# Kernel tuning notes

Hardware: AMD Instinct MI355X
Metric: run time of the kernel (lower is better)

Reference implementation:

```python
import jax, jax.numpy as jnp
import numpy as np

H, HD, CHUNK = 16, 64, 128


def _rotary(x):
    # x: (B,H,N,d); rotary_embedding_torch default: interleaved pairs, theta=10000
    N, d = x.shape[-2], x.shape[-1]
    inv_freq = 1.0 / (10000.0 ** (jnp.arange(0, d, 2, dtype=jnp.float32) / d))
    ang = jnp.arange(N, dtype=jnp.float32)[:, None] * inv_freq[None, :]  # (N, d/2)
    ang = jnp.repeat(ang, 2, axis=-1)  # (N, d), each freq repeated twice
    cos, sin = jnp.cos(ang), jnp.sin(ang)
    x1, x2 = x[..., 0::2], x[..., 1::2]
    xr = jnp.stack([-x2, x1], axis=-1).reshape(x.shape)  # rotate_half (interleaved)
    return x * cos + xr * sin


def _split_heads(t, B, N):
    return t.reshape(B, N, H, HD).transpose(0, 2, 1, 3)  # (B,H,N,Hd)


def _chunked(Q, KK, VK):
    # chunk-parallel linear-attention recurrence: per-token outer products,
    # intra-chunk cumsum, carried state across chunks, Frobenius normalization.
    B, h, N, d = Q.shape
    nc = N // CHUNK

    def to_chunks(t):
        return t.reshape(B, h, nc, CHUNK, d).transpose(2, 0, 1, 3, 4)  # (nc,B,h,c,d)

    S0 = jnp.eye(d, dtype=Q.dtype) * jnp.sqrt(jnp.float32(d))
    S0 = jnp.broadcast_to(S0, (B, h, d, d))

    def step(SK_state, inp):
        q, kk, vk = inp  # (B,h,c,d)
        ok = jnp.einsum('bhni,bhnj->bhnij', kk, vk)            # outer products
        SK = jnp.cumsum(ok, axis=2) + SK_state[:, :, None]      # prefix-sum + carry
        norm = jnp.sqrt(jnp.sum(SK * SK, axis=(-2, -1), keepdims=True)) + 1e-8
        SKn = SK / norm                                         # Frobenius-normalized
        y = jnp.einsum('bhni,bhnji->bhnj', q, SKn)              # q @ SK^T per token
        return SK[:, :, -1], y

    _, ys = jax.lax.scan(step, S0, (to_chunks(Q), to_chunks(KK), to_chunks(VK)))
    return ys.transpose(1, 2, 0, 3, 4).reshape(B, h, N, d)


def setup_inputs():
    key = jax.random.key(0)
    ks = jax.random.split(key, 5)
    B, N, D = 2, 2048, 1024
    X = jax.random.normal(ks[0], (B, N, D), jnp.float32)
    w_qkv = jax.random.normal(ks[1], (D, 3 * H * HD), jnp.float32) * 0.02
    w_kvkv = jax.random.normal(ks[2], (D, 4 * H * HD), jnp.float32) * 0.02
    w_out = jax.random.normal(ks[3], (H * HD, D), jnp.float32) * 0.02
    b_out = jnp.zeros((D,), jnp.float32)
    return {"X": X, "w_qkv": w_qkv, "w_kvkv": w_kvkv, "w_out": w_out, "b_out": b_out}


def reference(X, w_qkv, w_kvkv, w_out, b_out):
    B, N, D = X.shape
    q, k, v = jnp.split(X @ w_qkv, 3, axis=-1)
    Q = _split_heads(q, B, N)
    K = _split_heads(k, B, N)
    V = _split_heads(v, B, N)
    kk, vk, _kv, _vv = jnp.split(X @ w_kvkv, 4, axis=-1)
    KK = _split_heads(kk, B, N)
    VK = _split_heads(vk, B, N)
    # NOTE: the SV branch (KV, VV) in the original is returned by the chunked fn
    # but never used by forward's output, so it is dead code for the fwd result.
    Qn = _chunked(Q, KK, VK)
    Qr = _rotary(Qn)
    Kr = _rotary(K)
    scale = 1.0 / jnp.sqrt(jnp.float32(HD))
    scores = jnp.einsum('bhqd,bhkd->bhqk', Qr, Kr) * scale
    mask = jnp.tril(jnp.ones((N, N), dtype=bool))
    scores = jnp.where(mask, scores, -jnp.inf)
    attn = jax.nn.softmax(scores, axis=-1)
    out = jnp.einsum('bhqk,bhkd->bhqd', attn, V)
    out = out.transpose(0, 2, 1, 3).reshape(B, N, H * HD)
    return out @ w_out + b_out
```

## Files before the change

kernel.cpp:

```cpp
#include <hip/hip_runtime.h>

typedef unsigned int u32;
typedef unsigned short u16;
typedef __attribute__((ext_vector_type(8))) __bf16 bf16x8;
typedef __attribute__((ext_vector_type(4))) float f32x4;

constexpr int NH = 16;
constexpr int HDM = 64;
constexpr int NSQ = 2048;
constexpr int KD = 1024;
constexpr int BHT = 32;

__device__ __forceinline__ u16 f2bf(float f) {
  u32 u = __float_as_uint(f);
  u += 0x7fffu + ((u >> 16) & 1u);
  return (u16)(u >> 16);
}
__device__ __forceinline__ float bf2f(u16 h) {
  return __uint_as_float(((u32)h) << 16);
}

__device__ __forceinline__ void gl_lds16(const u16* g, u16* l) {
  __builtin_amdgcn_global_load_lds(
      (const __attribute__((address_space(1))) u32*)g,
      (__attribute__((address_space(3))) u32*)l, 16, 0, 0);
}

__device__ __forceinline__ bf16x8 ldf(const u16* b, int row, int cb, int rs) {
  return *(const bf16x8*)((const char*)b + row * rs + ((cb * 16) ^ ((row & 7) << 4)));
}

__global__ void k_f32_to_bf16(const float* __restrict__ src, u16* __restrict__ dst, int n4) {
  int i = blockIdx.x * 256 + threadIdx.x;
  if (i < n4) {
    float4 v = ((const float4*)src)[i];
    ushort4 o;
    o.x = f2bf(v.x); o.y = f2bf(v.y); o.z = f2bf(v.z); o.w = f2bf(v.w);
    ((ushort4*)dst)[i] = o;
  }
}

__global__ void k_transpose_bf16(const float* __restrict__ src, int srcld,
                                 u16* __restrict__ dst, int dstld) {
  __shared__ float tile[64][65];
  int ct = blockIdx.x * 64, kt = blockIdx.y * 64;
  int lc = threadIdx.x & 63, rg = threadIdx.x >> 6;
#pragma unroll
  for (int i = 0; i < 16; ++i) {
    int kl = rg * 16 + i;
    tile[kl][lc] = src[(size_t)(kt + kl) * srcld + ct + lc];
  }
  __syncthreads();
#pragma unroll
  for (int i = 0; i < 16; ++i) {
    int cl = rg * 16 + i;
    dst[(size_t)(ct + cl) * dstld + kt + lc] = f2bf(tile[lc][cl]);
  }
}

template <int MODE>
__device__ __forceinline__ void gemm_stage(const u16* __restrict__ A, const u16* __restrict__ Bt,
                                           u16* Albuf, u16* Blbuf, int mt, int nt, int kt,
                                           int w, int lane) {
#pragma unroll
  for (int i = 0; i < 2; ++i) {
    int ob = (w * 2 + i) * 1024 + lane * 16;
    int row = ob >> 6;
    int ke = (ob & 63) >> 1;
    const u16* ga;
    if (MODE == 0) {
      ga = A + (size_t)(mt * 128 + row) * KD + kt * 32 + ke;
    } else {
      int grow = mt * 128 + row;
      int k = kt * 32 + ke;
      ga = A + ((size_t)((grow >> 11) * NH + (k >> 6)) * NSQ + (grow & 2047)) * HDM + (k & 63);
    }
    gl_lds16(ga, Albuf + (w * 2 + i) * 512);
    const u16* gb = Bt + (size_t)(nt * 128 + row) * KD + kt * 32 + ke;
    gl_lds16(gb, Blbuf + (w * 2 + i) * 512);
  }
}

__device__ __forceinline__ void gemm_compute(const u16* Albuf, const u16* Blbuf,
                                             f32x4 acc[4][4], int wr, int wc, int g, int q) {
  bf16x8 af[4], bfr[4];
#pragma unroll
  for (int m = 0; m < 4; ++m)
    af[m] = *(const bf16x8*)(Albuf + (wr * 64 + m * 16 + q) * 32 + g * 8);
#pragma unroll
  for (int n = 0; n < 4; ++n)
    bfr[n] = *(const bf16x8*)(Blbuf + (wc * 64 + n * 16 + q) * 32 + g * 8);
#pragma unroll
  for (int m = 0; m < 4; ++m)
#pragma unroll
    for (int n = 0; n < 4; ++n)
      acc[m][n] = __builtin_amdgcn_mfma_f32_16x16x32_bf16(af[m], bfr[n], acc[m][n], 0, 0, 0);
}

template <int MODE>
__global__ __launch_bounds__(256) void k_gemm(const u16* __restrict__ A, const u16* __restrict__ Bt,
                                              u16* __restrict__ o0, u16* __restrict__ o1,
                                              u16* __restrict__ o2, u16* __restrict__ o3,
                                              u16* __restrict__ o4,
                                              const float* __restrict__ bias,
                                              float* __restrict__ Cout) {
  __shared__ __align__(16) u16 Al[2][4096];
  __shared__ __align__(16) u16 Bl[2][4096];
  int nt = blockIdx.x, mt = blockIdx.y;
  int tid = threadIdx.x, w = tid >> 6, lane = tid & 63;
  int g = lane >> 4, q = lane & 15, wr = w >> 1, wc = w & 1;
  f32x4 acc[4][4];
#pragma unroll
  for (int m = 0; m < 4; ++m)
#pragma unroll
    for (int n = 0; n < 4; ++n) acc[m][n] = (f32x4){0.f, 0.f, 0.f, 0.f};

  gemm_stage<MODE>(A, Bt, Al[0], Bl[0], mt, nt, 0, w, lane);
  __syncthreads();
  int cur = 0;
  for (int kt = 1; kt < 32; ++kt) {
    gemm_stage<MODE>(A, Bt, Al[cur ^ 1], Bl[cur ^ 1], mt, nt, kt, w, lane);
    gemm_compute(Al[cur], Bl[cur], acc, wr, wc, g, q);
    __syncthreads();
    cur ^= 1;
  }
  gemm_compute(Al[cur], Bl[cur], acc, wr, wc, g, q);

  if (MODE == 0) {
#pragma unroll
    for (int nf = 0; nf < 4; ++nf) {
      int c = nt * 128 + wc * 64 + nf * 16 + q;
      if (c >= 2048 && c < 3072) {
        int rem = c - 2048;
        int hh = rem >> 6, dd = rem & 63;
#pragma unroll
        for (int mf = 0; mf < 4; ++mf)
#pragma unroll
          for (int r = 0; r < 4; ++r) {
            int row = mt * 128 + wr * 64 + mf * 16 + g * 4 + r;
            int b = row >> 11, nn = row & 2047;
            o2[((size_t)(b * NH + hh) * HDM + dd) * NSQ + nn] = f2bf(acc[mf][nf][r]);
          }
      } else {
        u16* dst; int rem;
        if (c < 1024)      { dst = o0; rem = c; }
        else if (c < 2048) { dst = o1; rem = c - 1024; }
        else if (c < 4096) { dst = o3; rem = c - 3072; }
        else               { dst = o4; rem = c - 4096; }
        size_t hoff = (size_t)(rem >> 6) * NSQ * HDM + (rem & 63);
#pragma unroll
        for (int mf = 0; mf < 4; ++mf)
#pragma unroll
          for (int r = 0; r < 4; ++r) {
            int row = mt * 128 + wr * 64 + mf * 16 + g * 4 + r;
            int b = row >> 11, nn = row & 2047;
            dst[(size_t)b * NH * NSQ * HDM + hoff + (size_t)nn * HDM] = f2bf(acc[mf][nf][r]);
          }
      }
    }
  } else {
#pragma unroll
    for (int nf = 0; nf < 4; ++nf) {
      int c = nt * 128 + wc * 64 + nf * 16 + q;
      float bv = bias[c];
#pragma unroll
      for (int mf = 0; mf < 4; ++mf)
#pragma unroll
        for (int r = 0; r < 4; ++r) {
          int row = mt * 128 + wr * 64 + mf * 16 + g * 4 + r;
          Cout[(size_t)row * 1024 + c] = acc[mf][nf][r] + bv;
        }
    }
  }
}

__global__ void k_rotary(const u16* __restrict__ src, u16* __restrict__ dst, float scale) {
  int idx = blockIdx.x * 256 + threadIdx.x;
  if (idx >= BHT * NSQ * 32) return;
  int i = idx & 31;
  int n = (idx >> 5) & 2047;
  int bh = idx >> 16;
  float th = (float)n * exp2f(-(float)i * (13.287712379549449f / 32.0f));
  float s, c;
  sincosf(th, &s, &c);
  size_t base = ((size_t)bh * NSQ + n) * HDM + 2 * i;
  float x1 = bf2f(src[base]), x2 = bf2f(src[base + 1]);
  dst[base]     = f2bf((x1 * c - x2 * s) * scale);
  dst[base + 1] = f2bf((x2 * c + x1 * s) * scale);
}

__global__ __launch_bounds__(256) void k_chunk_outer(const u16* __restrict__ Kk,
                                                     const u16* __restrict__ Vk,
                                                     float* __restrict__ Mc) {
  int bhc = blockIdx.x;
  __shared__ float kk[128][64];
  __shared__ float vv[128][64];
  int tid = threadIdx.x;
  size_t base = ((size_t)(bhc >> 4) * NSQ + (size_t)(bhc & 15) * 128) * HDM;
  for (int i = tid; i < 2048; i += 256) {
    int r = i >> 4, c4 = (i & 15) * 4;
    ushort4 a = ((const ushort4*)(Kk + base))[i];
    kk[r][c4] = bf2f(a.x); kk[r][c4 + 1] = bf2f(a.y); kk[r][c4 + 2] = bf2f(a.z); kk[r][c4 + 3] = bf2f(a.w);
    ushort4 b = ((const ushort4*)(Vk + base))[i];
    vv[r][c4] = bf2f(b.x); vv[r][c4 + 1] = bf2f(b.y); vv[r][c4 + 2] = bf2f(b.z); vv[r][c4 + 3] = bf2f(b.w);
  }
  __syncthreads();
  int i0 = (tid >> 4) * 4, j0 = (tid & 15) * 4;
  float a2[4][4];
#pragma unroll
  for (int di = 0; di < 4; ++di)
#pragma unroll
    for (int dj = 0; dj < 4; ++dj) a2[di][dj] = 0.f;
  for (int m = 0; m < 128; ++m) {
    float ka[4], vb[4];
#pragma unroll
    for (int d = 0; d < 4; ++d) { ka[d] = kk[m][i0 + d]; vb[d] = vv[m][j0 + d]; }
#pragma unroll
    for (int di = 0; di < 4; ++di)
#pragma unroll
      for (int dj = 0; dj < 4; ++dj) a2[di][dj] += ka[di] * vb[dj];
  }
  float* out = Mc + (size_t)bhc * 4096;
#pragma unroll
  for (int di = 0; di < 4; ++di) {
    float4 v = make_float4(a2[di][0], a2[di][1], a2[di][2], a2[di][3]);
    *(float4*)(out + (i0 + di) * 64 + j0) = v;
  }
}

__global__ void k_chunk_prefix(const float* __restrict__ Mc, float* __restrict__ Sst) {
  int bh = blockIdx.x;
  int tid = threadIdx.x;
  int i0 = (tid >> 4) * 4, j0 = (tid & 15) * 4;
  float S[4][4];
#pragma unroll
  for (int di = 0; di < 4; ++di)
#pragma unroll
    for (int dj = 0; dj < 4; ++dj) S[di][dj] = ((i0 + di) == (j0 + dj)) ? 8.0f : 0.0f;
  for (int c = 0; c < 16; ++c) {
    size_t o = ((size_t)bh * 16 + c) * 4096;
#pragma unroll
    for (int di = 0; di < 4; ++di) {
      float4 v = make_float4(S[di][0], S[di][1], S[di][2], S[di][3]);
      *(float4*)(Sst + o + (i0 + di) * 64 + j0) = v;
      float4 mv = *(const float4*)(Mc + o + (i0 + di) * 64 + j0);
      S[di][0] += mv.x; S[di][1] += mv.y; S[di][2] += mv.z; S[di][3] += mv.w;
    }
  }
}

__global__ __launch_bounds__(256) void k_chunk_norm(const u16* __restrict__ Kk,
                                                    const u16* __restrict__ Vk,
                                                    const float* __restrict__ Sst,
                                                    float* __restrict__ Invn) {
  __shared__ __align__(16) u16 KkL[128 * 64];
  __shared__ __align__(16) u16 VkL[128 * 64];
  __shared__ __align__(16) u16 SL[64 * 64];
  __shared__ float prebuf[128][2];
  __shared__ float bilbuf[128][2];
  __shared__ float sc[128];
  __shared__ float red[4];
  int bhc = blockIdx.x;
  int tid = threadIdx.x, w = tid >> 6, lane = tid & 63;
  int g = lane >> 4, q = lane & 15;
  size_t base = (size_t)bhc * 8192;

  for (int ic = tid; ic < 1024; ic += 256) {
    int row = ic >> 3, cb = ic & 7;
    int off = row * 128 + ((cb * 16) ^ ((row & 7) << 4));
    *(uint4*)((char*)KkL + off) = ((const uint4*)(Kk + base))[ic];
    *(uint4*)((char*)VkL + off) = ((const uint4*)(Vk + base))[ic];
  }
  float ss = 0.f;
  const float4* Sg = (const float4*)(Sst + (size_t)bhc * 4096);
  for (int i = tid; i < 1024; i += 256) {
    float4 v = Sg[i];
    ss += v.x * v.x + v.y * v.y + v.z * v.z + v.w * v.w;
    int row = i >> 4, c8 = (i & 15) * 8;
    u32 lo = (u32)f2bf(v.x) | ((u32)f2bf(v.y) << 16);
    u32 hi = (u32)f2bf(v.z) | ((u32)f2bf(v.w) << 16);
    *(uint2*)((char*)SL + row * 128 + (c8 ^ ((row & 7) << 4))) = make_uint2(lo, hi);
  }
#pragma unroll
  for (int d = 1; d < 64; d <<= 1) ss += __shfl_xor(ss, d);
  if (lane == 0) red[w] = ss;
  __syncthreads();

  int wr = w >> 1, wc = w & 1;
  bf16x8 ka[4][2], va[4][2];
#pragma unroll
  for (int mf = 0; mf < 4; ++mf)
#pragma unroll
    for (int ks = 0; ks < 2; ++ks) {
      ka[mf][ks] = ldf(KkL, wr * 64 + mf * 16 + q, ks * 4 + g, 128);
      va[mf][ks] = ldf(VkL, wr * 64 + mf * 16 + q, ks * 4 + g, 128);
    }

  float pracc[4][4];
#pragma unroll
  for (int mf = 0; mf < 4; ++mf)
#pragma unroll
    for (int r = 0; r < 4; ++r) pracc[mf][r] = 0.f;
  for (int pf = 0; pf < 4; ++pf) {
    bf16x8 kb0 = ldf(KkL, wc * 64 + pf * 16 + q, g, 128);
    bf16x8 kb1 = ldf(KkL, wc * 64 + pf * 16 + q, 4 + g, 128);
    bf16x8 vb0 = ldf(VkL, wc * 64 + pf * 16 + q, g, 128);
    bf16x8 vb1 = ldf(VkL, wc * 64 + pf * 16 + q, 4 + g, 128);
#pragma unroll
    for (int mf = 0; mf < 4; ++mf) {
      f32x4 a1 = (f32x4){0.f, 0.f, 0.f, 0.f}, b1 = (f32x4){0.f, 0.f, 0.f, 0.f};
      a1 = __builtin_amdgcn_mfma_f32_16x16x32_bf16(ka[mf][0], kb0, a1, 0, 0, 0);
      a1 = __builtin_amdgcn_mfma_f32_16x16x32_bf16(ka[mf][1], kb1, a1, 0, 0, 0);
      b1 = __builtin_amdgcn_mfma_f32_16x16x32_bf16(va[mf][0], vb0, b1, 0, 0, 0);
      b1 = __builtin_amdgcn_mfma_f32_16x16x32_bf16(va[mf][1], vb1, b1, 0, 0, 0);
#pragma unroll
      for (int r = 0; r < 4; ++r) {
        int m = wr * 64 + mf * 16 + g * 4 + r;
        int p = wc * 64 + pf * 16 + q;
        float gv = a1[r] * b1[r];
        float coef = (p < m) ? 1.f : ((p == m) ? 0.5f : 0.f);
        pracc[mf][r] += coef * gv;
      }
    }
  }
#pragma unroll
  for (int mf = 0; mf < 4; ++mf)
#pragma unroll
    for (int r = 0; r < 4; ++r) {
      float v = pracc[mf][r];
      v += __shfl_xor(v, 1); v += __shfl_xor(v, 2); v += __shfl_xor(v, 4); v += __shfl_xor(v, 8);
      pracc[mf][r] = v;
    }
  if (q == 0) {
#pragma unroll
    for (int mf = 0; mf < 4; ++mf)
#pragma unroll
      for (int r = 0; r < 4; ++r) prebuf[wr * 64 + mf * 16 + g * 4 + r][wc] = pracc[mf][r];
  }

  float bacc[4][4];
#pragma unroll
  for (int mf = 0; mf < 4; ++mf)
#pragma unroll
    for (int r = 0; r < 4; ++r) bacc[mf][r] = 0.f;
  for (int jf = 0; jf < 2; ++jf) {
    bf16x8 sb0 = ldf(SL, wc * 32 + jf * 16 + q, g, 128);
    bf16x8 sb1 = ldf(SL, wc * 32 + jf * 16 + q, 4 + g, 128);
#pragma unroll
    for (int mf = 0; mf < 4; ++mf) {
      f32x4 u = (f32x4){0.f, 0.f, 0.f, 0.f};
      u = __builtin_amdgcn_mfma_f32_16x16x32_bf16(va[mf][0], sb0, u, 0, 0, 0);
      u = __builtin_amdgcn_mfma_f32_16x16x32_bf16(va[mf][1], sb1, u, 0, 0, 0);
#pragma unroll
      for (int r = 0; r < 4; ++r) {
        int m = wr * 64 + mf * 16 + g * 4 + r;
        int j = wc * 32 + jf * 16 + q;
        float kkv = bf2f(*(const u16*)((const char*)KkL + m * 128 + ((j * 2) ^ ((m & 7) << 4))));
        bacc[mf][r] += u[r] * kkv;
      }
    }
  }
#pragma unroll
  for (int mf = 0; mf < 4; ++mf)
#pragma unroll
    for (int r = 0; r < 4; ++r) {
      float v = bacc[mf][r];
      v += __shfl_xor(v, 1); v += __shfl_xor(v, 2); v += __shfl_xor(v, 4); v += __shfl_xor(v, 8);
      bacc[mf][r] = v;
    }
  if (q == 0) {
#pragma unroll
    for (int mf = 0; mf < 4; ++mf)
#pragma unroll
      for (int r = 0; r < 4; ++r) bilbuf[wr * 64 + mf * 16 + g * 4 + r][wc] = bacc[mf][r];
  }
  __syncthreads();

  if (tid < 128)
    sc[tid] = 2.f * (prebuf[tid][0] + prebuf[tid][1] + bilbuf[tid][0] + bilbuf[tid][1]);
  __syncthreads();
  for (int off = 1; off < 128; off <<= 1) {
    float add = 0.f;
    if (tid < 128 && tid >= off) add = sc[tid - off];
    __syncthreads();
    if (tid < 128) sc[tid] += add;
    __syncthreads();
  }
  if (tid < 128) {
    float n0 = red[0] + red[1] + red[2] + red[3];
    float cum = n0 + sc[tid];
    Invn[(size_t)bhc * 128 + tid] = 1.f / (sqrtf(cum) + 1e-8f);
  }
}

__global__ __launch_bounds__(256) void k_chunk_yv2(const u16* __restrict__ Qb,
                                                   const u16* __restrict__ Kk,
                                                   const u16* __restrict__ Vk,
                                                   const float* __restrict__ Sst,
                                                   const float* __restrict__ Invn,
                                                   u16* __restrict__ Qn) {
  __shared__ __align__(16) u16 QL[128 * 64];
  __shared__ __align__(16) u16 WL[128 * 64];
  __shared__ __align__(16) u16 SL[64 * 64];
  __shared__ __align__(16) u16 PL[128 * 128];
  __shared__ float inv[128];
  int bhc = blockIdx.x;
  int tid = threadIdx.x, w = tid >> 6, lane = tid & 63;
  int g = lane >> 4, q = lane & 15;
  size_t base = (size_t)bhc * 8192;

  for (int ic = tid; ic < 1024; ic += 256) {
    int row = ic >> 3, cb = ic & 7;
    int off = row * 128 + ((cb * 16) ^ ((row & 7) << 4));
    *(uint4*)((char*)QL + off) = ((const uint4*)(Qb + base))[ic];
    *(uint4*)((char*)WL + off) = ((const uint4*)(Vk + base))[ic];
  }
  const float4* Sg = (const float4*)(Sst + (size_t)bhc * 4096);
  for (int i = tid; i < 1024; i += 256) {
    float4 v = Sg[i];
    int row = i >> 4, c8 = (i & 15) * 8;
    u32 lo = (u32)f2bf(v.x) | ((u32)f2bf(v.y) << 16);
    u32 hi = (u32)f2bf(v.z) | ((u32)f2bf(v.w) << 16);
    *(uint2*)((char*)SL + row * 128 + (c8 ^ ((row & 7) << 4))) = make_uint2(lo, hi);
  }
  if (tid < 128) inv[tid] = Invn[(size_t)bhc * 128 + tid];
  __syncthreads();

  int wr = w >> 1, wc = w & 1;
  f32x4 pacc[4][4];
#pragma unroll
  for (int mf = 0; mf < 4; ++mf)
#pragma unroll
    for (int nf = 0; nf < 4; ++nf) pacc[mf][nf] = (f32x4){0.f, 0.f, 0.f, 0.f};
#pragma unroll
  for (int ks = 0; ks < 2; ++ks) {
    bf16x8 av[4], bq[4];
#pragma unroll
    for (int mf = 0; mf < 4; ++mf) av[mf] = ldf(WL, wr * 64 + mf * 16 + q, ks * 4 + g, 128);
#pragma unroll
    for (int nf = 0; nf < 4; ++nf) bq[nf] = ldf(QL, wc * 64 + nf * 16 + q, ks * 4 + g, 128);
#pragma unroll
    for (int mf = 0; mf < 4; ++mf)
#pragma unroll
      for (int nf = 0; nf < 4; ++nf)
        pacc[mf][nf] = __builtin_amdgcn_mfma_f32_16x16x32_bf16(av[mf], bq[nf], pacc[mf][nf], 0, 0, 0);
  }
#pragma unroll
  for (int mf = 0; mf < 4; ++mf)
#pragma unroll
    for (int nf = 0; nf < 4; ++nf) {
      int m0 = wr * 64 + mf * 16 + g * 4;
      int n = wc * 64 + nf * 16 + q;
      float v0 = (m0 + 0 <= n) ? pacc[mf][nf][0] : 0.f;
      float v1 = (m0 + 1 <= n) ? pacc[mf][nf][1] : 0.f;
      float v2 = (m0 + 2 <= n) ? pacc[mf][nf][2] : 0.f;
      float v3 = (m0 + 3 <= n) ? pacc[mf][nf][3] : 0.f;
      u32 lo = (u32)f2bf(v0) | ((u32)f2bf(v1) << 16);
      u32 hi = (u32)f2bf(v2) | ((u32)f2bf(v3) << 16);
      *(uint2*)((char*)PL + n * 256 + ((m0 * 2) ^ ((n & 7) << 4))) = make_uint2(lo, hi);
    }
  __syncthreads();
  for (int i = tid; i < 2048; i += 256) {
    int r = i >> 4, c4 = (i & 15) * 4;
    ushort4 kv = ((const ushort4*)(Kk + base))[i];
    *(u16*)((char*)WL + (c4 + 0) * 256 + ((r * 2) ^ (((c4 + 0) & 7) << 4))) = kv.x;
    *(u16*)((char*)WL + (c4 + 1) * 256 + ((r * 2) ^ (((c4 + 1) & 7) << 4))) = kv.y;
    *(u16*)((char*)WL + (c4 + 2) * 256 + ((r * 2) ^ (((c4 + 2) & 7) << 4))) = kv.z;
    *(u16*)((char*)WL + (c4 + 3) * 256 + ((r * 2) ^ (((c4 + 3) & 7) << 4))) = kv.w;
  }
  __syncthreads();

  f32x4 yacc[4][2];
#pragma unroll
  for (int nf = 0; nf < 4; ++nf)
#pragma unroll
    for (int jf = 0; jf < 2; ++jf) yacc[nf][jf] = (f32x4){0.f, 0.f, 0.f, 0.f};
#pragma unroll
  for (int ks = 0; ks < 2; ++ks) {
    bf16x8 aq[4], bs[2];
#pragma unroll
    for (int nf = 0; nf < 4; ++nf) aq[nf] = ldf(QL, wr * 64 + nf * 16 + q, ks * 4 + g, 128);
#pragma unroll
    for (int jf = 0; jf < 2; ++jf) bs[jf] = ldf(SL, wc * 32 + jf * 16 + q, ks * 4 + g, 128);
#pragma unroll
    for (int nf = 0; nf < 4; ++nf)
#pragma unroll
      for (int jf = 0; jf < 2; ++jf)
        yacc[nf][jf] = __builtin_amdgcn_mfma_f32_16x16x32_bf16(aq[nf], bs[jf], yacc[nf][jf], 0, 0, 0);
  }
#pragma unroll
  for (int ks = 0; ks < 4; ++ks) {
    bf16x8 ap[4], bk[2];
#pragma unroll
    for (int nf = 0; nf < 4; ++nf) ap[nf] = ldf(PL, wr * 64 + nf * 16 + q, ks * 4 + g, 256);
#pragma unroll
    for (int jf = 0; jf < 2; ++jf) bk[jf] = ldf(WL, wc * 32 + jf * 16 + q, ks * 4 + g, 256);
#pragma unroll
    for (int nf = 0; nf < 4; ++nf)
#pragma unroll
      for (int jf = 0; jf < 2; ++jf)
        yacc[nf][jf] = __builtin_amdgcn_mfma_f32_16x16x32_bf16(ap[nf], bk[jf], yacc[nf][jf], 0, 0, 0);
  }
#pragma unroll
  for (int nf = 0; nf < 4; ++nf)
#pragma unroll
    for (int jf = 0; jf < 2; ++jf)
#pragma unroll
      for (int r = 0; r < 4; ++r) {
        int n = wr * 64 + nf * 16 + g * 4 + r;
        int j = wc * 32 + jf * 16 + q;
        Qn[base + (size_t)n * 64 + j] = f2bf(yacc[nf][jf][r] * inv[n]);
      }
}

__global__ __launch_bounds__(512) void k_attn2(const u16* __restrict__ Qr, const u16* __restrict__ Kr,
                                               const u16* __restrict__ Vt, u16* __restrict__ Ob) {
  __shared__ __align__(16) u16 QL[128 * 64];
  __shared__ __align__(16) u16 KL[2][64 * 64];
  __shared__ __align__(16) u16 VL[2][64 * 64];
  __shared__ __align__(16) u16 PLa[8][16 * 64];
  int bh = blockIdx.x, pair = blockIdx.y;
  int tid = threadIdx.x, w = tid >> 6, lane = tid & 63;
  int g = lane >> 4, q16 = lane & 15;
  const u16* Qg_base = Qr + (size_t)bh * NSQ * HDM;
  const u16* Kg_base = Kr + (size_t)bh * NSQ * HDM;
  const u16* VTg_base = Vt + (size_t)bh * HDM * NSQ;
  u16* Og_base = Ob + (size_t)bh * NSQ * HDM;
  u16* Pw = PLa[w];
  int srow = tid >> 3, scb = tid & 7;

  for (int phase = 0; phase < 2; ++phase) {
    int t = phase ? (15 - pair) : pair;
    int qbase = t * 128;
    int nkt = 2 * t + 2;
    int lastkt_w = (qbase + w * 16 + 15) >> 6;
    int qg_ = qbase + w * 16 + q16;

    {
      const u16* Qg = Qg_base + qbase * 64;
#pragma unroll
      for (int it = 0; it < 2; ++it) {
        int c = it * 512 + tid;
        int row = c >> 3, cb = c & 7;
        gl_lds16(Qg + row * 64 + ((cb ^ (row & 7)) << 3), QL + c * 8);
      }
    }
    gl_lds16(Kg_base + srow * 64 + ((scb ^ (srow & 7)) << 3), KL[0] + tid * 8);
    gl_lds16(VTg_base + (size_t)srow * NSQ + ((scb ^ (srow & 7)) << 3), VL[0] + tid * 8);
    __syncthreads();

    bf16x8 qf[2];
    qf[0] = ldf(QL, w * 16 + q16, g, 128);
    qf[1] = ldf(QL, w * 16 + q16, 4 + g, 128);

    f32x4 o[4];
#pragma unroll
    for (int df = 0; df < 4; ++df) o[df] = (f32x4){0.f, 0.f, 0.f, 0.f};
    float m_run = -3.0e38f, l_run = 0.f;

    int cur = 0;
    for (int kt = 0; kt < nkt; ++kt) {
      if (kt + 1 < nkt) {
        gl_lds16(Kg_base + (kt + 1) * 4096 + srow * 64 + ((scb ^ (srow & 7)) << 3),
                 KL[cur ^ 1] + tid * 8);
        gl_lds16(VTg_base + (size_t)srow * NSQ + (kt + 1) * 64 + ((scb ^ (srow & 7)) << 3),
                 VL[cur ^ 1] + tid * 8);
      }
      if (kt <= lastkt_w) {
        const u16* Kbuf = KL[cur];
        const u16* Vbuf = VL[cur];
        f32x4 st[4];
#pragma unroll
        for (int kf = 0; kf < 4; ++kf) {
          f32x4 s = (f32x4){0.f, 0.f, 0.f, 0.f};
          s = __builtin_amdgcn_mfma_f32_16x16x32_bf16(ldf(Kbuf, kf * 16 + q16, g, 128), qf[0], s, 0, 0, 0);
          s = __builtin_amdgcn_mfma_f32_16x16x32_bf16(ldf(Kbuf, kf * 16 + q16, 4 + g, 128), qf[1], s, 0, 0, 0);
          st[kf] = s;
        }
        float smax = -1e30f;
        bool needmask = (kt * 64 + 63 > qbase + w * 16);
        if (needmask) {
#pragma unroll
          for (int kf = 0; kf < 4; ++kf)
#pragma unroll
            for (int r = 0; r < 4; ++r) {
              int keyg = kt * 64 + kf * 16 + g * 4 + r;
              float sv = st[kf][r];
              sv = (keyg <= qg_) ? sv : -1e30f;
              st[kf][r] = sv;
              smax = fmaxf(smax, sv);
            }
        } else {
#pragma unroll
          for (int kf = 0; kf < 4; ++kf)
#pragma unroll
            for (int r = 0; r < 4; ++r) smax = fmaxf(smax, st[kf][r]);
        }
        smax = fmaxf(smax, __shfl_xor(smax, 16));
        smax = fmaxf(smax, __shfl_xor(smax, 32));
        float mnew = fmaxf(m_run, smax);
        float corr = __expf(m_run - mnew);
        float ls = 0.f;
#pragma unroll
        for (int kf = 0; kf < 4; ++kf)
#pragma unroll
          for (int r = 0; r < 4; ++r) {
            float p = __expf(st[kf][r] - mnew);
            st[kf][r] = p;
            ls += p;
          }
        ls += __shfl_xor(ls, 16);
        ls += __shfl_xor(ls, 32);
        m_run = mnew;
        l_run = l_run * corr + ls;
#pragma unroll
        for (int df = 0; df < 4; ++df) {
          o[df][0] *= corr; o[df][1] *= corr; o[df][2] *= corr; o[df][3] *= corr;
        }
#pragma unroll
        for (int kf = 0; kf < 4; ++kf) {
          u32 lo = (u32)f2bf(st[kf][0]) | ((u32)f2bf(st[kf][1]) << 16);
          u32 hi = (u32)f2bf(st[kf][2]) | ((u32)f2bf(st[kf][3]) << 16);
          int ba = q16 * 128 + ((kf * 32 + g * 8) ^ ((q16 & 7) << 4));
          *(u32*)((char*)Pw + ba) = lo;
          *(u32*)((char*)Pw + ba + 4) = hi;
        }
#pragma unroll
        for (int kc = 0; kc < 2; ++kc) {
          bf16x8 pf = ldf(Pw, q16, kc * 4 + g, 128);
#pragma unroll
          for (int df = 0; df < 4; ++df) {
            bf16x8 vf = ldf(Vbuf, df * 16 + q16, kc * 4 + g, 128);
            o[df] = __builtin_amdgcn_mfma_f32_16x16x32_bf16(vf, pf, o[df], 0, 0, 0);
          }
        }
      }
      __syncthreads();
      cur ^= 1;
    }
    float invl = 1.0f / l_run;
    u16* Og = Og_base + (size_t)(qbase + w * 16 + q16) * HDM;
#pragma unroll
    for (int df = 0; df < 4; ++df)
#pragma unroll
      for (int r = 0; r < 4; ++r) Og[df * 16 + g * 4 + r] = f2bf(o[df][r] * invl);
  }
}

extern "C" void kernel_launch(void* const* d_in, const int* in_sizes, int n_in,
                              void* d_out, int out_size, void* d_ws, size_t ws_size,
                              hipStream_t stream) {
  const float* X = (const float*)d_in[0];
  const float* w_qkv = (const float*)d_in[1];
  const float* w_kvkv = (const float*)d_in[2];
  const float* w_out = (const float*)d_in[3];
  const float* b_out = (const float*)d_in[4];
  float* out = (float*)d_out;
  char* ws = (char*)d_ws;

  u16* Xb  = (u16*)(ws + 0);
  u16* WbT = (u16*)(ws + 8388608);
  u16* WoT = (u16*)(ws + 18874368);
  u16* Qb  = (u16*)(ws + 20971520);
  u16* Kb  = (u16*)(ws + 29360128);
  u16* Vtb = (u16*)(ws + 37748736);
  u16* Kkb = (u16*)(ws + 46137344);
  u16* Vkb = (u16*)(ws + 54525952);
  u16* Kr  = (u16*)(ws + 62914560);
  u16* Qr  = (u16*)(ws + 71303168);
  float* Mc   = (float*)(ws + 8388608);
  float* Invn = (float*)(ws + 16777216);
  float* Sst  = (float*)(ws + 29360128);
  u16* Ob = (u16*)(ws + 0);
  (void)in_sizes; (void)n_in; (void)out_size; (void)ws_size;

  k_f32_to_bf16<<<dim3(4096), dim3(256), 0, stream>>>(X, Xb, 1048576);
  k_transpose_bf16<<<dim3(48, 16), dim3(256), 0, stream>>>(w_qkv, 3072, WbT, 1024);
  k_transpose_bf16<<<dim3(32, 16), dim3(256), 0, stream>>>(w_kvkv, 4096, WbT + (size_t)3072 * 1024, 1024);
  k_transpose_bf16<<<dim3(16, 16), dim3(256), 0, stream>>>(w_out, 1024, WoT, 1024);
  k_gemm<0><<<dim3(40, 32), dim3(256), 0, stream>>>(Xb, WbT, Qb, Kb, Vtb, Kkb, Vkb, nullptr, nullptr);
  k_rotary<<<dim3(8192), dim3(256), 0, stream>>>(Kb, Kr, 1.0f);
  k_chunk_outer<<<dim3(512), dim3(256), 0, stream>>>(Kkb, Vkb, Mc);
  k_chunk_prefix<<<dim3(32), dim3(256), 0, stream>>>(Mc, Sst);
  k_chunk_norm<<<dim3(512), dim3(256), 0, stream>>>(Kkb, Vkb, Sst, Invn);
  k_chunk_yv2<<<dim3(512), dim3(256), 0, stream>>>(Qb, Kkb, Vkb, Sst, Invn, Qb);
  k_rotary<<<dim3(8192), dim3(256), 0, stream>>>(Qb, Qr, 0.125f);
  k_attn2<<<dim3(32, 8), dim3(512), 0, stream>>>(Qr, Kr, Vtb, Ob);
  k_gemm<1><<<dim3(8, 32), dim3(256), 0, stream>>>(Ob, WoT, nullptr, nullptr, nullptr, nullptr, nullptr, b_out, out);
}
```

Measured before the change: 207.0 us.

## Fuse rotary embedding into GEMM and chunk epilogues; widen prefix-scan grid

Applies the rotary embedding for K directly in the projection GEMM epilogue, and for Q (with the 1/8 scale) in the chunked linear-attention output epilogue. Each lane gets its interleaved partner value through a lane xor-1 shuffle. This removes two standalone rotary kernels and their extra bf16 round trips through memory. The chunk prefix kernel is also split across 8 row groups per head so it uses more blocks. The fused paths add sincos work inside the epilogues and depend on adjacent columns sitting in adjacent lanes.

```diff
diff --git a/kernel.cpp b/kernel.cpp
--- a/kernel.cpp
+++ b/kernel.cpp
@@ -10,6 +10,7 @@
 constexpr int NSQ = 2048;
 constexpr int KD = 1024;
 constexpr int BHT = 32;
+constexpr float ROT_C = 13.287712379549449f / 32.0f;
 
 __device__ __forceinline__ u16 f2bf(float f) {
   u32 u = __float_as_uint(f);
@@ -130,7 +131,25 @@
 #pragma unroll
     for (int nf = 0; nf < 4; ++nf) {
       int c = nt * 128 + wc * 64 + nf * 16 + q;
-      if (c >= 2048 && c < 3072) {
+      if (c >= 1024 && c < 2048) {
+        int rem = c - 1024;
+        int hh = rem >> 6, dd = rem & 63;
+        float invf = exp2f(-(float)(dd >> 1) * ROT_C);
+        float sgn = (dd & 1) ? 1.0f : -1.0f;
+        size_t hoff = (size_t)hh * NSQ * HDM + dd;
+#pragma unroll
+        for (int mf = 0; mf < 4; ++mf)
+#pragma unroll
+          for (int r = 0; r < 4; ++r) {
+            int row = mt * 128 + wr * 64 + mf * 16 + g * 4 + r;
+            int b = row >> 11, nn = row & 2047;
+            float mine = acc[mf][nf][r];
+            float part = __shfl_xor(mine, 1);
+            float s, cc;
+            sincosf((float)nn * invf, &s, &cc);
+            o1[(size_t)b * NH * NSQ * HDM + hoff + (size_t)nn * HDM] = f2bf(mine * cc + sgn * part * s);
+          }
+      } else if (c >= 2048 && c < 3072) {
         int rem = c - 2048;
         int hh = rem >> 6, dd = rem & 63;
 #pragma unroll
@@ -144,7 +163,6 @@
       } else {
         u16* dst; int rem;
         if (c < 1024)      { dst = o0; rem = c; }
-        else if (c < 2048) { dst = o1; rem = c - 1024; }
         else if (c < 4096) { dst = o3; rem = c - 3072; }
         else               { dst = o4; rem = c - 4096; }
         size_t hoff = (size_t)(rem >> 6) * NSQ * HDM + (rem & 63);
@@ -172,21 +190,6 @@
         }
     }
   }
-}
-
-__global__ void k_rotary(const u16* __restrict__ src, u16* __restrict__ dst, float scale) {
-  int idx = blockIdx.x * 256 + threadIdx.x;
-  if (idx >= BHT * NSQ * 32) return;
-  int i = idx & 31;
-  int n = (idx >> 5) & 2047;
-  int bh = idx >> 16;
-  float th = (float)n * exp2f(-(float)i * (13.287712379549449f / 32.0f));
-  float s, c;
-  sincosf(th, &s, &c);
-  size_t base = ((size_t)bh * NSQ + n) * HDM + 2 * i;
-  float x1 = bf2f(src[base]), x2 = bf2f(src[base + 1]);
-  dst[base]     = f2bf((x1 * c - x2 * s) * scale);
-  dst[base + 1] = f2bf((x2 * c + x1 * s) * scale);
 }
 
 __global__ __launch_bounds__(256) void k_chunk_outer(const u16* __restrict__ Kk,
@@ -228,24 +231,20 @@
   }
 }
 
-__global__ void k_chunk_prefix(const float* __restrict__ Mc, float* __restrict__ Sst) {
-  int bh = blockIdx.x;
+__global__ __launch_bounds__(256) void k_chunk_prefix2(const float* __restrict__ Mc,
+                                                       float* __restrict__ Sst) {
+  int bh = blockIdx.x, rg = blockIdx.y;
   int tid = threadIdx.x;
-  int i0 = (tid >> 4) * 4, j0 = (tid & 15) * 4;
-  float S[4][4];
-#pragma unroll
-  for (int di = 0; di < 4; ++di)
-#pragma unroll
-    for (int dj = 0; dj < 4; ++dj) S[di][dj] = ((i0 + di) == (j0 + dj)) ? 8.0f : 0.0f;
+  int r8 = tid >> 5, cp = tid & 31;
+  int i = rg * 8 + r8, j0 = cp * 2;
+  float s0 = (i == j0) ? 8.0f : 0.0f;
+  float s1 = (i == j0 + 1) ? 8.0f : 0.0f;
+  size_t rowoff = (size_t)i * 64 + j0;
   for (int c = 0; c < 16; ++c) {
-    size_t o = ((size_t)bh * 16 + c) * 4096;
-#pragma unroll
-    for (int di = 0; di < 4; ++di) {
-      float4 v = make_float4(S[di][0], S[di][1], S[di][2], S[di][3]);
-      *(float4*)(Sst + o + (i0 + di) * 64 + j0) = v;
-      float4 mv = *(const float4*)(Mc + o + (i0 + di) * 64 + j0);
-      S[di][0] += mv.x; S[di][1] += mv.y; S[di][2] += mv.z; S[di][3] += mv.w;
-    }
+    size_t o = ((size_t)bh * 16 + c) * 4096 + rowoff;
+    *(float2*)(Sst + o) = make_float2(s0, s1);
+    float2 mv = *(const float2*)(Mc + o);
+    s0 += mv.x; s1 += mv.y;
   }
 }
 
@@ -398,7 +397,7 @@
                                                    const u16* __restrict__ Vk,
                                                    const float* __restrict__ Sst,
                                                    const float* __restrict__ Invn,
-                                                   u16* __restrict__ Qn) {
+                                                   u16* __restrict__ Qro) {
   __shared__ __align__(16) u16 QL[128 * 64];
   __shared__ __align__(16) u16 WL[128 * 64];
   __shared__ __align__(16) u16 SL[64 * 64];
@@ -504,13 +503,21 @@
 #pragma unroll
   for (int nf = 0; nf < 4; ++nf)
 #pragma unroll
-    for (int jf = 0; jf < 2; ++jf)
+    for (int jf = 0; jf < 2; ++jf) {
+      int j = wc * 32 + jf * 16 + q;
+      float invf = exp2f(-(float)(j >> 1) * ROT_C);
+      float sgn = (j & 1) ? 1.0f : -1.0f;
 #pragma unroll
       for (int r = 0; r < 4; ++r) {
         int n = wr * 64 + nf * 16 + g * 4 + r;
-        int j = wc * 32 + jf * 16 + q;
-        Qn[base + (size_t)n * 64 + j] = f2bf(yacc[nf][jf][r] * inv[n]);
+        float val = yacc[nf][jf][r] * inv[n];
+        float part = __shfl_xor(val, 1);
+        int ng = (bhc & 15) * 128 + n;
+        float s, cc;
+        sincosf((float)ng * invf, &s, &cc);
+        Qro[base + (size_t)n * 64 + j] = f2bf((val * cc + sgn * part * s) * 0.125f);
       }
+    }
 }
 
 __global__ __launch_bounds__(512) void k_attn2(const u16* __restrict__ Qr, const u16* __restrict__ Kr,
@@ -662,7 +669,7 @@
   u16* WbT = (u16*)(ws + 8388608);
   u16* WoT = (u16*)(ws + 18874368);
   u16* Qb  = (u16*)(ws + 20971520);
-  u16* Kb  = (u16*)(ws + 29360128);
+  float* Sst = (float*)(ws + 29360128);
   u16* Vtb = (u16*)(ws + 37748736);
   u16* Kkb = (u16*)(ws + 46137344);
   u16* Vkb = (u16*)(ws + 54525952);
@@ -670,7 +677,6 @@
   u16* Qr  = (u16*)(ws + 71303168);
   float* Mc   = (float*)(ws + 8388608);
   float* Invn = (float*)(ws + 16777216);
-  float* Sst  = (float*)(ws + 29360128);
   u16* Ob = (u16*)(ws + 0);
   (void)in_sizes; (void)n_in; (void)out_size; (void)ws_size;
 
@@ -678,13 +684,11 @@
   k_transpose_bf16<<<dim3(48, 16), dim3(256), 0, stream>>>(w_qkv, 3072, WbT, 1024);
   k_transpose_bf16<<<dim3(32, 16), dim3(256), 0, stream>>>(w_kvkv, 4096, WbT + (size_t)3072 * 1024, 1024);
   k_transpose_bf16<<<dim3(16, 16), dim3(256), 0, stream>>>(w_out, 1024, WoT, 1024);
-  k_gemm<0><<<dim3(40, 32), dim3(256), 0, stream>>>(Xb, WbT, Qb, Kb, Vtb, Kkb, Vkb, nullptr, nullptr);
-  k_rotary<<<dim3(8192), dim3(256), 0, stream>>>(Kb, Kr, 1.0f);
+  k_gemm<0><<<dim3(40, 32), dim3(256), 0, stream>>>(Xb, WbT, Qb, Kr, Vtb, Kkb, Vkb, nullptr, nullptr);
   k_chunk_outer<<<dim3(512), dim3(256), 0, stream>>>(Kkb, Vkb, Mc);
-  k_chunk_prefix<<<dim3(32), dim3(256), 0, stream>>>(Mc, Sst);
+  k_chunk_prefix2<<<dim3(32, 8), dim3(256), 0, stream>>>(Mc, Sst);
   k_chunk_norm<<<dim3(512), dim3(256), 0, stream>>>(Kkb, Vkb, Sst, Invn);
-  k_chunk_yv2<<<dim3(512), dim3(256), 0, stream>>>(Qb, Kkb, Vkb, Sst, Invn, Qb);
-  k_rotary<<<dim3(8192), dim3(256), 0, stream>>>(Qb, Qr, 0.125f);
+  k_chunk_yv2<<<dim3(512), dim3(256), 0, stream>>>(Qb, Kkb, Vkb, Sst, Invn, Qr);
   k_attn2<<<dim3(32, 8), dim3(512), 0, stream>>>(Qr, Kr, Vtb, Ob);
   k_gemm<1><<<dim3(8, 32), dim3(256), 0, stream>>>(Ob, WoT, nullptr, nullptr, nullptr, nullptr, nullptr, b_out, out);
 }
```

Result: slower. 544.1 us (+162.8%).
